# Optimization experiments

Hardware: AMD Instinct MI355X
Metric: run time of the kernel (lower is better)

Reference implementation:

```python
import jax, jax.numpy as jnp
import numpy as np

NUM_HEADS = 6


def setup_inputs() -> dict:
    key = jax.random.key(0)
    k1, k2, k3 = jax.random.split(key, 3)
    b_, n, c = 512, 256, 192
    nw = 64
    x = jax.random.normal(k1, (b_, n, c), dtype=jnp.float32)
    mask = jnp.zeros((nw, n, n), dtype=jnp.float32)  # 0 / -inf additive window mask
    W_qkv = jax.random.normal(k2, (3 * c, c), dtype=jnp.float32) * 0.02
    W_proj = jax.random.normal(k3, (c, c), dtype=jnp.float32) * 0.02
    b_proj = jnp.zeros((c,), dtype=jnp.float32)
    return {"x": x, "mask": mask, "W_qkv": W_qkv, "W_proj": W_proj, "b_proj": b_proj}


def reference(x, mask, W_qkv, W_proj, b_proj):
    b_, n, c = x.shape
    h = NUM_HEADS
    d = c // h
    scale = d ** (-0.5)
    # qkv projection (no bias): (b_, n, 3, h, d) -> (3, b_, h, n, d)
    qkv = (x @ W_qkv.T).reshape(b_, n, 3, h, d).transpose(2, 0, 3, 1, 4)
    q, k, v = qkv[0], qkv[1], qkv[2]
    q = q * scale
    attn = jnp.einsum('bhid,bhjd->bhij', q, k)  # (b_, h, n, n)
    nw = mask.shape[0]
    # add per-window mask bias: view as (B, nw, h, n, n) + (1, nw, 1, n, n)
    attn = attn.reshape(b_ // nw, nw, h, n, n) + mask[None, :, None, :, :]
    attn = attn.reshape(b_, h, n, n)
    attn = jax.nn.softmax(attn, axis=-1)
    out = jnp.einsum('bhij,bhjd->bhid', attn, v)  # (b_, h, n, d)
    out = out.transpose(0, 2, 1, 3).reshape(b_, n, c)
    return out @ W_proj.T + b_proj
```

## Files before the change

### kernel.cpp

```cpp
#include <hip/hip_runtime.h>
#include <hip/hip_bf16.h>
#include <stdint.h>

typedef short bf16x8 __attribute__((ext_vector_type(8)));
typedef float f32x4 __attribute__((ext_vector_type(4)));

#define B_   512
#define N_   256
#define C_   192
#define H_   6
#define D_   32
#define NW_  64

__device__ __forceinline__ uint16_t f2bf(float f) {
    uint32_t u = __builtin_bit_cast(uint32_t, f);
    u += 0x7FFFu + ((u >> 16) & 1u);
    return (uint16_t)(u >> 16);
}

__device__ __forceinline__ uint32_t pk_bf16(float a, float b) {
    float2 t; t.x = a; t.y = b;
    __hip_bfloat162 h = __float22bfloat162_rn(t);
    uint32_t u;
    __builtin_memcpy(&u, &h, 4);
    return u;
}

__device__ __forceinline__ bf16x8 ld_bf8(const uint16_t* p) {
    uint4 u = *reinterpret_cast<const uint4*>(p);
    return __builtin_bit_cast(bf16x8, u);
}

__global__ void prep_kernel(const float* __restrict__ mask,
                            const float* __restrict__ wqkv,
                            const float* __restrict__ wproj,
                            uint16_t* __restrict__ sel,
                            uint16_t* __restrict__ wqkv_bf,
                            uint16_t* __restrict__ wproj_bf) {
    const int64_t NSEL = (int64_t)NW_ * N_ * N_;
    const int64_t NWQ  = 3 * C_ * C_;
    const int64_t NWP  = (int64_t)C_ * C_;
    int64_t i = (int64_t)blockIdx.x * blockDim.x + threadIdx.x;
    int64_t stride = (int64_t)gridDim.x * blockDim.x;
    for (; i < NSEL + NWQ + NWP; i += stride) {
        if (i < NSEL) {
            sel[i] = (mask[i] == 0.0f) ? 0xFFFFu : 0u;
        } else if (i < NSEL + NWQ) {
            int64_t j = i - NSEL;
            wqkv_bf[j] = f2bf(wqkv[j]);
        } else {
            int64_t j = i - NSEL - NWQ;
            wproj_bf[j] = f2bf(wproj[j]);
        }
    }
}

#define SA 200
#define SB 72
__global__ __launch_bounds__(512, 4)
void qkv_kernel(const float* __restrict__ x, const uint16_t* __restrict__ wq,
                uint16_t* __restrict__ qbuf, uint16_t* __restrict__ kbuf,
                uint16_t* __restrict__ vtbuf) {
    __shared__ __align__(16) uint16_t Alds[128 * SA];
    __shared__ __align__(16) uint16_t Blds[192 * SB];
    const int tid  = threadIdx.x;
    const int lane = tid & 63;
    const int wv   = tid >> 6;
    const int wrow = wv >> 2;
    const int wcol = wv & 3;
    const int quad = lane >> 4;
    const int l15  = lane & 15;
    const int m0   = blockIdx.x * 128;

#pragma unroll
    for (int p = 0; p < 12; p++) {
        int f = p * 512 + tid;
        int row = f / 48, c4 = f % 48;
        const float4 v = *reinterpret_cast<const float4*>(
            x + (int64_t)(m0 + row) * 192 + c4 * 4);
        uint2 d;
        d.x = pk_bf16(v.x, v.y);
        d.y = pk_bf16(v.z, v.w);
        *reinterpret_cast<uint2*>(&Alds[row * SA + c4 * 4]) = d;
    }

    const float scale = 0.17677669529663687f;

    for (int cb = 0; cb < 3; cb++) {
        f32x4 acc[4][3];
#pragma unroll
        for (int i = 0; i < 4; i++)
#pragma unroll
            for (int j = 0; j < 3; j++) acc[i][j] = (f32x4)0.f;

        for (int k0 = 0; k0 < 192; k0 += 64) {
            __syncthreads();
#pragma unroll
            for (int p = 0; p < 3; p++) {
                int u = p * 512 + tid;
                int row = u >> 3, c8 = u & 7;
                uint4 w = *reinterpret_cast<const uint4*>(
                    wq + (int64_t)(cb * 192 + row) * 192 + k0 + c8 * 8);
                *reinterpret_cast<uint4*>(&Blds[row * SB + c8 * 8]) = w;
            }
            __syncthreads();
#pragma unroll
            for (int ks = 0; ks < 2; ks++) {
                bf16x8 xf[4], wf[3];
#pragma unroll
                for (int i = 0; i < 4; i++)
                    xf[i] = *reinterpret_cast<const bf16x8*>(
                        &Alds[(wrow * 64 + i * 16 + l15) * SA + k0 + ks * 32 + quad * 8]);
#pragma unroll
                for (int j = 0; j < 3; j++)
                    wf[j] = *reinterpret_cast<const bf16x8*>(
                        &Blds[(wcol * 48 + j * 16 + l15) * SB + ks * 32 + quad * 8]);
                if (cb < 2) {
#pragma unroll
                    for (int i = 0; i < 4; i++)
#pragma unroll
                        for (int j = 0; j < 3; j++)
                            acc[i][j] = __builtin_amdgcn_mfma_f32_16x16x32_bf16(
                                wf[j], xf[i], acc[i][j], 0, 0, 0);
                } else {
#pragma unroll
                    for (int i = 0; i < 4; i++)
#pragma unroll
                        for (int j = 0; j < 3; j++)
                            acc[i][j] = __builtin_amdgcn_mfma_f32_16x16x32_bf16(
                                xf[i], wf[j], acc[i][j], 0, 0, 0);
                }
            }
        }

        if (cb < 2) {
            uint16_t* dst = (cb == 0) ? qbuf : kbuf;
            const float sc = (cb == 0) ? scale : 1.0f;
#pragma unroll
            for (int i = 0; i < 4; i++) {
                int m = m0 + wrow * 64 + i * 16 + l15;
                int b = m >> 8, pos = m & 255;
#pragma unroll
                for (int j = 0; j < 3; j++) {
                    int cbase = wcol * 48 + j * 16 + quad * 4;
                    int h = cbase >> 5, d0 = cbase & 31;
                    int64_t bh = (int64_t)b * H_ + h;
                    uint2 s;
                    s.x = pk_bf16(acc[i][j][0] * sc, acc[i][j][1] * sc);
                    s.y = pk_bf16(acc[i][j][2] * sc, acc[i][j][3] * sc);
                    *reinterpret_cast<uint2*>(&dst[(bh * N_ + pos) * D_ + d0]) = s;
                }
            }
        } else {
#pragma unroll
            for (int i = 0; i < 4; i++) {
                int m = m0 + wrow * 64 + i * 16 + quad * 4;
                int b = m >> 8, pos0 = m & 255;
#pragma unroll
                for (int j = 0; j < 3; j++) {
                    int c = wcol * 48 + j * 16 + l15;
                    int h = c >> 5, d = c & 31;
                    int64_t bh = (int64_t)b * H_ + h;
                    uint2 s;
                    s.x = pk_bf16(acc[i][j][0], acc[i][j][1]);
                    s.y = pk_bf16(acc[i][j][2], acc[i][j][3]);
                    *reinterpret_cast<uint2*>(&vtbuf[(bh * D_ + d) * N_ + pos0]) = s;
                }
            }
        }
    }
}

__global__ __launch_bounds__(256, 2)
void attn_kernel(const uint16_t* __restrict__ qbuf, const uint16_t* __restrict__ kbuf,
                 const uint16_t* __restrict__ vtbuf, const uint16_t* __restrict__ sel,
                 uint16_t* __restrict__ aout) {
    __shared__ __align__(16) uint16_t Plds[4 * 64 * 72];
    const int bi = blockIdx.x;
    const int h  = bi % 6;
    const int g  = (bi / 6) & 7;
    const int w  = bi / 48;
    const int b  = g * 64 + w;
    const int tid  = threadIdx.x;
    const int lane = tid & 63;
    const int wv   = tid >> 6;
    const int quad = lane >> 4;
    const int l15  = lane & 15;
    const int i0   = wv * 64;
    const int64_t bh = (int64_t)b * H_ + h;
    const uint16_t* qB = qbuf  + bh * N_ * D_;
    const uint16_t* kB = kbuf  + bh * N_ * D_;
    const uint16_t* vB = vtbuf + bh * D_ * N_;
    const uint16_t* sB = sel   + (int64_t)w * N_ * N_;
    uint16_t* Pw = &Plds[wv * 64 * 72];

    bf16x8 qf[4];
#pragma unroll
    for (int it = 0; it < 4; it++)
        qf[it] = ld_bf8(&qB[(i0 + it * 16 + l15) * D_ + quad * 8]);

    f32x4 oacc[4][2];
    f32x4 lacc[4];
#pragma unroll
    for (int mt = 0; mt < 4; mt++) {
        oacc[mt][0] = (f32x4)0.f; oacc[mt][1] = (f32x4)0.f; lacc[mt] = (f32x4)0.f;
    }
    bf16x8 ones;
#pragma unroll
    for (int e = 0; e < 8; e++) ones[e] = (short)0x3F80;

    for (int jc = 0; jc < 4; jc++) {
        const int j0 = jc * 64;
        bf16x8 kf[4];
#pragma unroll
        for (int jt = 0; jt < 4; jt++)
            kf[jt] = ld_bf8(&kB[(j0 + jt * 16 + l15) * D_ + quad * 8]);

        f32x4 sacc[4][4];
#pragma unroll
        for (int jt = 0; jt < 4; jt++)
#pragma unroll
            for (int it = 0; it < 4; it++) sacc[jt][it] = (f32x4)0.f;
#pragma unroll
        for (int jt = 0; jt < 4; jt++)
#pragma unroll
            for (int it = 0; it < 4; it++)
                sacc[jt][it] = __builtin_amdgcn_mfma_f32_16x16x32_bf16(
                    kf[jt], qf[it], sacc[jt][it], 0, 0, 0);

#pragma unroll
        for (int it = 0; it < 4; it++)
#pragma unroll
            for (int jt = 0; jt < 4; jt++) {
                f32x4 s = sacc[jt][it];
                uint2 d;
                d.x = pk_bf16(__expf(s[0]), __expf(s[1]));
                d.y = pk_bf16(__expf(s[2]), __expf(s[3]));
                *reinterpret_cast<uint2*>(
                    &Pw[(it * 16 + l15) * 72 + jt * 16 + quad * 4]) = d;
            }

        bf16x8 vf[2][2];
#pragma unroll
        for (int ks = 0; ks < 2; ks++)
#pragma unroll
            for (int nt = 0; nt < 2; nt++)
                vf[ks][nt] = ld_bf8(&vB[(nt * 16 + l15) * N_ + j0 + ks * 32 + quad * 8]);

#pragma unroll
        for (int ks = 0; ks < 2; ks++)
#pragma unroll
            for (int mt = 0; mt < 4; mt++) {
                uint4 p = *reinterpret_cast<const uint4*>(
                    &Pw[(mt * 16 + l15) * 72 + ks * 32 + quad * 8]);
                const uint4 s = *reinterpret_cast<const uint4*>(
                    &sB[(int64_t)(i0 + mt * 16 + l15) * N_ + j0 + ks * 32 + quad * 8]);
                p.x &= s.x; p.y &= s.y; p.z &= s.z; p.w &= s.w;
                bf16x8 pa = __builtin_bit_cast(bf16x8, p);
                oacc[mt][0] = __builtin_amdgcn_mfma_f32_16x16x32_bf16(pa, vf[ks][0], oacc[mt][0], 0, 0, 0);
                oacc[mt][1] = __builtin_amdgcn_mfma_f32_16x16x32_bf16(pa, vf[ks][1], oacc[mt][1], 0, 0, 0);
                lacc[mt]    = __builtin_amdgcn_mfma_f32_16x16x32_bf16(pa, ones,      lacc[mt],    0, 0, 0);
            }
    }

#pragma unroll
    for (int mt = 0; mt < 4; mt++)
#pragma unroll
        for (int r = 0; r < 4; r++) {
            float inv = 1.0f / lacc[mt][r];
            int i = i0 + mt * 16 + quad * 4 + r;
#pragma unroll
            for (int nt = 0; nt < 2; nt++) {
                float v = oacc[mt][nt][r] * inv;
                aout[((int64_t)b * N_ + i) * C_ + h * 32 + nt * 16 + l15] = f2bf(v);
            }
        }
}

__global__ __launch_bounds__(512, 2)
void proj_kernel(const uint16_t* __restrict__ a, const uint16_t* __restrict__ wp,
                 const float* __restrict__ bias, float* __restrict__ out) {
    __shared__ __align__(16) uint16_t Alds[128 * 72];
    __shared__ __align__(16) uint16_t Blds[192 * 72];
    const int tid  = threadIdx.x;
    const int lane = tid & 63;
    const int wv   = tid >> 6;
    const int wm   = wv >> 2;
    const int wn   = wv & 3;
    const int quad = lane >> 4;
    const int l15  = lane & 15;
    const int m0   = blockIdx.x * 128;

    f32x4 acc[4][3];
#pragma unroll
    for (int x = 0; x < 4; x++)
#pragma unroll
        for (int y = 0; y < 3; y++) acc[x][y] = (f32x4)0.f;

    for (int k0 = 0; k0 < 192; k0 += 64) {
        __syncthreads();
#pragma unroll
        for (int p = 0; p < 2; p++) {
            int u = tid + p * 512;
            int row = u >> 3, c8 = u & 7;
            uint4 v = *reinterpret_cast<const uint4*>(
                a + (int64_t)(m0 + row) * 192 + k0 + c8 * 8);
            *reinterpret_cast<uint4*>(&Alds[row * 72 + c8 * 8]) = v;
        }
#pragma unroll
        for (int p = 0; p < 3; p++) {
            int u = tid + p * 512;
            int row = u >> 3, c8 = u & 7;
            uint4 v = *reinterpret_cast<const uint4*>(
                wp + (int64_t)row * 192 + k0 + c8 * 8);
            *reinterpret_cast<uint4*>(&Blds[row * 72 + c8 * 8]) = v;
        }
        __syncthreads();
#pragma unroll
        for (int ks = 0; ks < 2; ks++) {
            bf16x8 af[4], bfr[3];
#pragma unroll
            for (int mt = 0; mt < 4; mt++)
                af[mt] = *reinterpret_cast<const bf16x8*>(
                    &Alds[(wm * 64 + mt * 16 + l15) * 72 + ks * 32 + quad * 8]);
#pragma unroll
            for (int nt = 0; nt < 3; nt++)
                bfr[nt] = *reinterpret_cast<const bf16x8*>(
                    &Blds[(wn * 48 + nt * 16 + l15) * 72 + ks * 32 + quad * 8]);
#pragma unroll
            for (int mt = 0; mt < 4; mt++)
#pragma unroll
                for (int nt = 0; nt < 3; nt++)
                    acc[mt][nt] = __builtin_amdgcn_mfma_f32_16x16x32_bf16(
                        af[mt], bfr[nt], acc[mt][nt], 0, 0, 0);
        }
    }
    float bv[3];
#pragma unroll
    for (int nt = 0; nt < 3; nt++) bv[nt] = bias[wn * 48 + nt * 16 + l15];
#pragma unroll
    for (int mt = 0; mt < 4; mt++)
#pragma unroll
        for (int r = 0; r < 4; r++) {
            int m = m0 + wm * 64 + mt * 16 + quad * 4 + r;
#pragma unroll
            for (int nt = 0; nt < 3; nt++) {
                int col = wn * 48 + nt * 16 + l15;
                out[(int64_t)m * 192 + col] = acc[mt][nt][r] + bv[nt];
            }
        }
}

extern "C" void kernel_launch(void* const* d_in, const int* in_sizes, int n_in,
                              void* d_out, int out_size, void* d_ws, size_t ws_size,
                              hipStream_t stream) {
    const float* x     = (const float*)d_in[0];
    const float* mask  = (const float*)d_in[1];
    const float* wqkv  = (const float*)d_in[2];
    const float* wproj = (const float*)d_in[3];
    const float* bproj = (const float*)d_in[4];
    float* out = (float*)d_out;

    uint16_t* qbuf = (uint16_t*)d_out;
    uint16_t* kbuf = qbuf + 25165824;
    char* ws = (char*)d_ws;
    uint16_t* vtbuf = (uint16_t*)(ws);
    uint16_t* aout  = (uint16_t*)(ws + 50331648);
    uint16_t* sel   = (uint16_t*)(ws + 100663296);
    uint16_t* wq_bf = (uint16_t*)(ws + 109051904);
    uint16_t* wp_bf = (uint16_t*)(ws + 109273088);

    prep_kernel<<<4096, 256, 0, stream>>>(mask, wqkv, wproj, sel, wq_bf, wp_bf);
    qkv_kernel<<<1024, 512, 0, stream>>>(x, wq_bf, qbuf, kbuf, vtbuf);
    attn_kernel<<<3072, 256, 0, stream>>>(qbuf, kbuf, vtbuf, sel, aout);
    proj_kernel<<<1024, 512, 0, stream>>>(aout, wp_bf, bproj, out);
}
```

Before: 356.2 us.

## Split attention rows across blocks, skip mask loads when mask is all-zero, use exp2

Attention blocks now handle 128 query rows instead of 256, doubling the grid and raising the occupancy target to 3 blocks per SM with a smaller LDS P buffer. The prep kernel sets a device flag when any mask entry is nonzero, and the attention kernel skips reading the select mask when the flag is clear. log2(e) is folded into the Q scale so the exponent uses exp2. K fragments are prefetched one chunk ahead, and MFMA sections are wrapped in s_setprio. The mask check is computed at runtime on device, so nonzero masks are still handled correctly. It adds a memset and an atomic to each call.

```diff
diff --git a/kernel.cpp b/kernel.cpp
--- a/kernel.cpp
+++ b/kernel.cpp
@@ -36,15 +36,19 @@
                             const float* __restrict__ wproj,
                             uint16_t* __restrict__ sel,
                             uint16_t* __restrict__ wqkv_bf,
-                            uint16_t* __restrict__ wproj_bf) {
+                            uint16_t* __restrict__ wproj_bf,
+                            unsigned* __restrict__ flag) {
     const int64_t NSEL = (int64_t)NW_ * N_ * N_;
     const int64_t NWQ  = 3 * C_ * C_;
     const int64_t NWP  = (int64_t)C_ * C_;
     int64_t i = (int64_t)blockIdx.x * blockDim.x + threadIdx.x;
     int64_t stride = (int64_t)gridDim.x * blockDim.x;
+    bool nz = false;
     for (; i < NSEL + NWQ + NWP; i += stride) {
         if (i < NSEL) {
-            sel[i] = (mask[i] == 0.0f) ? 0xFFFFu : 0u;
+            float m = mask[i];
+            nz |= (m != 0.0f);
+            sel[i] = (m == 0.0f) ? 0xFFFFu : 0u;
         } else if (i < NSEL + NWQ) {
             int64_t j = i - NSEL;
             wqkv_bf[j] = f2bf(wqkv[j]);
@@ -53,6 +57,8 @@
             wproj_bf[j] = f2bf(wproj[j]);
         }
     }
+    if (flag && __any(nz) && ((threadIdx.x & 63) == 0))
+        atomicOr(flag, 1u);
 }
 
 #define SA 200
@@ -84,7 +90,7 @@
         *reinterpret_cast<uint2*>(&Alds[row * SA + c4 * 4]) = d;
     }
 
-    const float scale = 0.17677669529663687f;
+    const float scale = 0.17677669529663687f * 1.4426950408889634f;
 
     for (int cb = 0; cb < 3; cb++) {
         f32x4 acc[4][3];
@@ -171,107 +177,147 @@
     }
 }
 
-__global__ __launch_bounds__(256, 2)
+__global__ __launch_bounds__(256, 3)
 void attn_kernel(const uint16_t* __restrict__ qbuf, const uint16_t* __restrict__ kbuf,
                  const uint16_t* __restrict__ vtbuf, const uint16_t* __restrict__ sel,
+                 const unsigned* __restrict__ flag,
                  uint16_t* __restrict__ aout) {
-    __shared__ __align__(16) uint16_t Plds[4 * 64 * 72];
+    __shared__ __align__(16) uint16_t Plds[4 * 2 * 32 * 40];
     const int bi = blockIdx.x;
     const int h  = bi % 6;
-    const int g  = (bi / 6) & 7;
-    const int w  = bi / 48;
+    const int r_ = bi / 6;
+    const int ih = r_ & 1;
+    const int g  = (r_ >> 1) & 7;
+    const int w  = r_ >> 4;
     const int b  = g * 64 + w;
     const int tid  = threadIdx.x;
     const int lane = tid & 63;
     const int wv   = tid >> 6;
     const int quad = lane >> 4;
     const int l15  = lane & 15;
-    const int i0   = wv * 64;
+    const int i0   = ih * 128 + wv * 32;
+    const bool hasmask = flag ? (*flag != 0u) : true;
     const int64_t bh = (int64_t)b * H_ + h;
     const uint16_t* qB = qbuf  + bh * N_ * D_;
     const uint16_t* kB = kbuf  + bh * N_ * D_;
     const uint16_t* vB = vtbuf + bh * D_ * N_;
     const uint16_t* sB = sel   + (int64_t)w * N_ * N_;
-    uint16_t* Pw = &Plds[wv * 64 * 72];
-
-    bf16x8 qf[4];
-#pragma unroll
-    for (int it = 0; it < 4; it++)
+    uint16_t* Pw = &Plds[wv * 2 * 32 * 40];
+
+    bf16x8 qf[2];
+#pragma unroll
+    for (int it = 0; it < 2; it++)
         qf[it] = ld_bf8(&qB[(i0 + it * 16 + l15) * D_ + quad * 8]);
 
-    f32x4 oacc[4][2];
-    f32x4 lacc[4];
-#pragma unroll
-    for (int mt = 0; mt < 4; mt++) {
+    f32x4 oacc[2][2];
+    f32x4 lacc[2];
+#pragma unroll
+    for (int mt = 0; mt < 2; mt++) {
         oacc[mt][0] = (f32x4)0.f; oacc[mt][1] = (f32x4)0.f; lacc[mt] = (f32x4)0.f;
     }
     bf16x8 ones;
 #pragma unroll
     for (int e = 0; e < 8; e++) ones[e] = (short)0x3F80;
+
+    bf16x8 kf[4];
+#pragma unroll
+    for (int jt = 0; jt < 4; jt++)
+        kf[jt] = ld_bf8(&kB[(jt * 16 + l15) * D_ + quad * 8]);
 
     for (int jc = 0; jc < 4; jc++) {
         const int j0 = jc * 64;
-        bf16x8 kf[4];
-#pragma unroll
-        for (int jt = 0; jt < 4; jt++)
-            kf[jt] = ld_bf8(&kB[(j0 + jt * 16 + l15) * D_ + quad * 8]);
-
-        f32x4 sacc[4][4];
-#pragma unroll
-        for (int jt = 0; jt < 4; jt++)
-#pragma unroll
-            for (int it = 0; it < 4; it++) sacc[jt][it] = (f32x4)0.f;
-#pragma unroll
-        for (int jt = 0; jt < 4; jt++)
-#pragma unroll
-            for (int it = 0; it < 4; it++)
-                sacc[jt][it] = __builtin_amdgcn_mfma_f32_16x16x32_bf16(
-                    kf[jt], qf[it], sacc[jt][it], 0, 0, 0);
-
-#pragma unroll
-        for (int it = 0; it < 4; it++)
-#pragma unroll
-            for (int jt = 0; jt < 4; jt++) {
-                f32x4 s = sacc[jt][it];
-                uint2 d;
-                d.x = pk_bf16(__expf(s[0]), __expf(s[1]));
-                d.y = pk_bf16(__expf(s[2]), __expf(s[3]));
-                *reinterpret_cast<uint2*>(
-                    &Pw[(it * 16 + l15) * 72 + jt * 16 + quad * 4]) = d;
-            }
+
+        bf16x8 kfn[4];
+        if (jc < 3) {
+#pragma unroll
+            for (int jt = 0; jt < 4; jt++)
+                kfn[jt] = ld_bf8(&kB[(j0 + 64 + jt * 16 + l15) * D_ + quad * 8]);
+        }
 
         bf16x8 vf[2][2];
 #pragma unroll
-        for (int ks = 0; ks < 2; ks++)
+        for (int hf = 0; hf < 2; hf++)
 #pragma unroll
             for (int nt = 0; nt < 2; nt++)
-                vf[ks][nt] = ld_bf8(&vB[(nt * 16 + l15) * N_ + j0 + ks * 32 + quad * 8]);
-
-#pragma unroll
-        for (int ks = 0; ks < 2; ks++)
-#pragma unroll
-            for (int mt = 0; mt < 4; mt++) {
+                vf[hf][nt] = ld_bf8(&vB[(nt * 16 + l15) * N_ + j0 + hf * 32 + quad * 8]);
+
+        uint4 sv[2][2];
+        if (hasmask) {
+#pragma unroll
+            for (int hf = 0; hf < 2; hf++)
+#pragma unroll
+                for (int mt = 0; mt < 2; mt++)
+                    sv[hf][mt] = *reinterpret_cast<const uint4*>(
+                        &sB[(int64_t)(i0 + mt * 16 + l15) * N_ + j0 + hf * 32 + quad * 8]);
+        } else {
+#pragma unroll
+            for (int hf = 0; hf < 2; hf++)
+#pragma unroll
+                for (int mt = 0; mt < 2; mt++)
+                    sv[hf][mt] = make_uint4(~0u, ~0u, ~0u, ~0u);
+        }
+
+#pragma unroll
+        for (int hf = 0; hf < 2; hf++) {
+            f32x4 sacc[2][2];
+#pragma unroll
+            for (int jt2 = 0; jt2 < 2; jt2++)
+#pragma unroll
+                for (int it = 0; it < 2; it++) sacc[jt2][it] = (f32x4)0.f;
+            __builtin_amdgcn_s_setprio(1);
+#pragma unroll
+            for (int jt2 = 0; jt2 < 2; jt2++)
+#pragma unroll
+                for (int it = 0; it < 2; it++)
+                    sacc[jt2][it] = __builtin_amdgcn_mfma_f32_16x16x32_bf16(
+                        kf[hf * 2 + jt2], qf[it], sacc[jt2][it], 0, 0, 0);
+            __builtin_amdgcn_s_setprio(0);
+
+            uint16_t* Ph = Pw + hf * (32 * 40);
+#pragma unroll
+            for (int it = 0; it < 2; it++)
+#pragma unroll
+                for (int jt2 = 0; jt2 < 2; jt2++) {
+                    f32x4 s = sacc[jt2][it];
+                    uint2 d;
+                    d.x = pk_bf16(__builtin_amdgcn_exp2f(s[0]),
+                                  __builtin_amdgcn_exp2f(s[1]));
+                    d.y = pk_bf16(__builtin_amdgcn_exp2f(s[2]),
+                                  __builtin_amdgcn_exp2f(s[3]));
+                    *reinterpret_cast<uint2*>(
+                        &Ph[(it * 16 + l15) * 40 + jt2 * 16 + quad * 4]) = d;
+                }
+
+#pragma unroll
+            for (int mt = 0; mt < 2; mt++) {
                 uint4 p = *reinterpret_cast<const uint4*>(
-                    &Pw[(mt * 16 + l15) * 72 + ks * 32 + quad * 8]);
-                const uint4 s = *reinterpret_cast<const uint4*>(
-                    &sB[(int64_t)(i0 + mt * 16 + l15) * N_ + j0 + ks * 32 + quad * 8]);
-                p.x &= s.x; p.y &= s.y; p.z &= s.z; p.w &= s.w;
+                    &Ph[(mt * 16 + l15) * 40 + quad * 8]);
+                p.x &= sv[hf][mt].x; p.y &= sv[hf][mt].y;
+                p.z &= sv[hf][mt].z; p.w &= sv[hf][mt].w;
                 bf16x8 pa = __builtin_bit_cast(bf16x8, p);
-                oacc[mt][0] = __builtin_amdgcn_mfma_f32_16x16x32_bf16(pa, vf[ks][0], oacc[mt][0], 0, 0, 0);
-                oacc[mt][1] = __builtin_amdgcn_mfma_f32_16x16x32_bf16(pa, vf[ks][1], oacc[mt][1], 0, 0, 0);
+                __builtin_amdgcn_s_setprio(1);
+                oacc[mt][0] = __builtin_amdgcn_mfma_f32_16x16x32_bf16(pa, vf[hf][0], oacc[mt][0], 0, 0, 0);
+                oacc[mt][1] = __builtin_amdgcn_mfma_f32_16x16x32_bf16(pa, vf[hf][1], oacc[mt][1], 0, 0, 0);
                 lacc[mt]    = __builtin_amdgcn_mfma_f32_16x16x32_bf16(pa, ones,      lacc[mt],    0, 0, 0);
-            }
-    }
-
-#pragma unroll
-    for (int mt = 0; mt < 4; mt++)
-#pragma unroll
-        for (int r = 0; r < 4; r++) {
-            float inv = 1.0f / lacc[mt][r];
-            int i = i0 + mt * 16 + quad * 4 + r;
+                __builtin_amdgcn_s_setprio(0);
+            }
+        }
+
+        if (jc < 3) {
+#pragma unroll
+            for (int jt = 0; jt < 4; jt++) kf[jt] = kfn[jt];
+        }
+    }
+
+#pragma unroll
+    for (int mt = 0; mt < 2; mt++)
+#pragma unroll
+        for (int r4 = 0; r4 < 4; r4++) {
+            float inv = 1.0f / lacc[mt][r4];
+            int i = i0 + mt * 16 + quad * 4 + r4;
 #pragma unroll
             for (int nt = 0; nt < 2; nt++) {
-                float v = oacc[mt][nt][r] * inv;
+                float v = oacc[mt][nt][r4] * inv;
                 aout[((int64_t)b * N_ + i) * C_ + h * 32 + nt * 16 + l15] = f2bf(v);
             }
         }
@@ -369,9 +415,13 @@
     uint16_t* sel   = (uint16_t*)(ws + 100663296);
     uint16_t* wq_bf = (uint16_t*)(ws + 109051904);
     uint16_t* wp_bf = (uint16_t*)(ws + 109273088);
-
-    prep_kernel<<<4096, 256, 0, stream>>>(mask, wqkv, wproj, sel, wq_bf, wp_bf);
+    unsigned* flag  = nullptr;
+    if (ws_size >= 109346816 + 4)
+        flag = (unsigned*)(ws + 109346816);
+
+    if (flag) hipMemsetAsync(flag, 0, 4, stream);
+    prep_kernel<<<4096, 256, 0, stream>>>(mask, wqkv, wproj, sel, wq_bf, wp_bf, flag);
     qkv_kernel<<<1024, 512, 0, stream>>>(x, wq_bf, qbuf, kbuf, vtbuf);
-    attn_kernel<<<3072, 256, 0, stream>>>(qbuf, kbuf, vtbuf, sel, aout);
+    attn_kernel<<<6144, 256, 0, stream>>>(qbuf, kbuf, vtbuf, sel, flag, aout);
     proj_kernel<<<1024, 512, 0, stream>>>(aout, wp_bf, bproj, out);
 }
```

After: 325.5 us. -8.6%, faster.
